# Optimization experiments

Measured on AMD Instinct MI355X. Metric: run time of the kernel, lower is better.

Reference implementation:

```python
import jax, jax.numpy as jnp
import numpy as np

KS, STRIDE, DIL = 5, 1, 1
PAD = (KS + (KS - 1) * (DIL - 1) - 1) // 2
EPS = 1e-5


def _unfold_t(x):
    # x: (N, C, T, V) -> (N, C, T_out, KS, V), zero-padded temporal windows
    N, C, T, V = x.shape
    xp = jnp.pad(x, ((0, 0), (0, 0), (PAD, PAD), (0, 0)))
    t_out = (T + 2 * PAD - DIL * (KS - 1) - 1) // STRIDE + 1
    idx = jnp.arange(t_out)[:, None] * STRIDE + jnp.arange(KS)[None, :] * DIL  # (T_out, KS)
    return xp[:, :, idx, :]


def _bn2d(x, g, b):
    # training-mode BatchNorm2d: biased batch stats over (N, T, V)
    mu = jnp.mean(x, axis=(0, 2, 3), keepdims=True)
    var = jnp.var(x, axis=(0, 2, 3), keepdims=True)
    xn = (x - mu) * jax.lax.rsqrt(var + EPS)
    return xn * g[None, :, None, None] + b[None, :, None, None]


def setup_inputs() -> dict:
    key = jax.random.key(0)
    ks = jax.random.split(key, 8)
    N, C, T, V = 64, 64, 128, 25
    R, O = 8, 128
    s = 0.05
    return {
        "x": jax.random.normal(ks[0], (N, C, T, V), jnp.float32),
        "Wv": jax.random.normal(ks[1], (R, C), jnp.float32) * s,
        "bv": jax.random.normal(ks[2], (R,), jnp.float32) * s,
        "Ww": jax.random.normal(ks[3], (KS * KS, KS), jnp.float32) * s,
        "bw": jax.random.normal(ks[4], (KS * KS,), jnp.float32) * s,
        "g_bn": jnp.ones((R,), jnp.float32),
        "b_bn": jnp.zeros((R,), jnp.float32),
        "Wr": jax.random.normal(ks[5], (R, C), jnp.float32) * s,
        "br": jax.random.normal(ks[6], (R,), jnp.float32) * s,
        "g_r": jnp.ones((R,), jnp.float32),
        "b_r": jnp.zeros((R,), jnp.float32),
        "Wo": jax.random.normal(ks[7], (O, R), jnp.float32) * s,
        "bo": jnp.zeros((O,), jnp.float32),
        "g_o": jnp.ones((O,), jnp.float32),
        "b_o": jnp.zeros((O,), jnp.float32),
    }


def reference(x, Wv, bv, Ww, bw, g_bn, b_bn, Wr, br, g_r, b_r, Wo, bo, g_o, b_o):
    N, C, T, V = x.shape
    # convV (1x1) then unfold both x and v
    v0 = jnp.einsum('rc,nctv->nrtv', Wv, x) + bv[None, :, None, None]
    xu = _unfold_t(x)      # (N, C, T, W, V)
    vu = _unfold_t(v0)     # (N, R, T, W, V)
    # mean over channels, move window dim to channel position for convW
    m = jnp.mean(xu, axis=1).transpose(0, 2, 1, 3)  # (N, W, T, V)
    w = jnp.einsum('ow,nwtv->notv', Ww, m) + bw[None, :, None, None]
    weights = jnp.tanh(w.reshape(N, KS, KS, T, V))  # (N, W, W, T, V)
    att = jnp.einsum('nwutv,nctuv->nctv', weights, vu)  # (N, R, T, V)
    # residual 1x1 conv + BN (in_channels != out_channels -> conv path)
    res = _bn2d(jnp.einsum('rc,nctv->nrtv', Wr, x) + br[None, :, None, None], g_r, b_r)
    h = _bn2d(att, g_bn, b_bn) + res
    h = jnp.where(h >= 0, h, 0.1 * h)  # LeakyReLU(0.1)
    out = _bn2d(jnp.einsum('or,nrtv->notv', Wo, h) + bo[None, :, None, None], g_o, b_o)
    return out
```

## Files before the change

kernel.cpp:

```cpp
#include <hip/hip_runtime.h>
#include <math.h>

#define TV 3200
#define NTV 204800
#define NB 400
constexpr float EPSF = 1e-5f;

template<int NS>
__device__ inline void partials2(const float (&vals)[NS], float* lds, float* out, int ncols){
  int lane = threadIdx.x & 63, wid = threadIdx.x >> 6;
  #pragma unroll
  for (int j = 0; j < NS; ++j){
    float v = vals[j];
    #pragma unroll
    for (int o = 32; o > 0; o >>= 1) v += __shfl_down(v, o);
    if (lane == 0) lds[j*2 + wid] = v;
  }
  __syncthreads();
  if ((int)threadIdx.x < NS)
    out[threadIdx.x*ncols + blockIdx.x] = lds[threadIdx.x*2] + lds[threadIdx.x*2 + 1];
}

__global__ __launch_bounds__(128, 2) void k_proj(
    const float* __restrict__ x, const float* __restrict__ Wv, const float* __restrict__ bv,
    const float* __restrict__ Wr, const float* __restrict__ br,
    float* __restrict__ v0, float* __restrict__ r0, float* __restrict__ s,
    float* __restrict__ pr){
  __shared__ __align__(16) float sW[1024];
  __shared__ float lds[32];
  const int tid = threadIdx.x;
  for (int i = tid; i < 1024; i += 128){
    int c = i >> 4, j = i & 15;
    sW[i] = (j < 8) ? Wv[j*64 + c] : Wr[(j-8)*64 + c];
  }
  __syncthreads();
  const int p4 = (blockIdx.x*128 + tid) * 4;
  const int n = p4 / TV, tv4 = p4 - n*TV;
  const float* xb = x + (size_t)n*64*TV + tv4;
  float4 av[8], ar[8];
  #pragma unroll
  for (int r = 0; r < 8; ++r){
    av[r] = make_float4(0.f,0.f,0.f,0.f);
    ar[r] = make_float4(0.f,0.f,0.f,0.f);
  }
  float4 ss = make_float4(0.f,0.f,0.f,0.f);
  #pragma unroll 8
  for (int c = 0; c < 64; ++c){
    float4 xv = *(const float4*)(xb + (size_t)c*TV);
    ss.x += xv.x; ss.y += xv.y; ss.z += xv.z; ss.w += xv.w;
    #pragma unroll
    for (int r = 0; r < 8; ++r){
      float wv = sW[c*16 + r], wr = sW[c*16 + 8 + r];
      av[r].x = fmaf(wv, xv.x, av[r].x); av[r].y = fmaf(wv, xv.y, av[r].y);
      av[r].z = fmaf(wv, xv.z, av[r].z); av[r].w = fmaf(wv, xv.w, av[r].w);
      ar[r].x = fmaf(wr, xv.x, ar[r].x); ar[r].y = fmaf(wr, xv.y, ar[r].y);
      ar[r].z = fmaf(wr, xv.z, ar[r].z); ar[r].w = fmaf(wr, xv.w, ar[r].w);
    }
  }
  *(float4*)(s + p4) = make_float4(ss.x*0.015625f, ss.y*0.015625f, ss.z*0.015625f, ss.w*0.015625f);
  float vals[16];
  #pragma unroll
  for (int r = 0; r < 8; ++r){
    float bvr = bv[r], brr = br[r];
    float4 vv = make_float4(av[r].x+bvr, av[r].y+bvr, av[r].z+bvr, av[r].w+bvr);
    *(float4*)(v0 + (size_t)r*NTV + p4) = vv;
    float4 rr = make_float4(ar[r].x+brr, ar[r].y+brr, ar[r].z+brr, ar[r].w+brr);
    *(float4*)(r0 + (size_t)r*NTV + p4) = rr;
    vals[r]   = rr.x + rr.y + rr.z + rr.w;
    vals[8+r] = rr.x*rr.x + rr.y*rr.y + rr.z*rr.z + rr.w*rr.w;
  }
  partials2<16>(vals, lds, pr, NB);
}

__global__ __launch_bounds__(128, 2) void k_att(
    const float* __restrict__ s, const float* __restrict__ Ww, const float* __restrict__ bw,
    const float* __restrict__ v0, float* __restrict__ att, float* __restrict__ patt){
  __shared__ __align__(16) float sS[616];
  __shared__ __align__(16) float sV[8*616];
  __shared__ float sWw[128], sbw[32];
  __shared__ float lds[32];
  const int tid = threadIdx.x;
  if (tid < 125) sWw[tid] = Ww[tid];
  if (tid < 25)  sbw[tid] = bw[tid];
  const int P0 = blockIdx.x * 512;
  const int base = P0 - 52;
  for (int i = tid; i < 154; i += 128){
    int q = base + i*4;
    float4 val;
    if (q >= 0 && q + 3 < NTV) val = *(const float4*)(s + q);
    else {
      float tmp[4];
      #pragma unroll
      for (int j = 0; j < 4; ++j){ int qe = q + j; tmp[j] = (qe >= 0 && qe < NTV) ? s[qe] : 0.f; }
      val = make_float4(tmp[0], tmp[1], tmp[2], tmp[3]);
    }
    *(float4*)&sS[i*4] = val;
  }
  for (int i = tid; i < 1232; i += 128){
    int r = i / 154, j = i - r*154;
    int q = base + j*4;
    const float* vr = v0 + (size_t)r*NTV;
    float4 val;
    if (q >= 0 && q + 3 < NTV) val = *(const float4*)(vr + q);
    else {
      float tmp[4];
      #pragma unroll
      for (int jj = 0; jj < 4; ++jj){ int qe = q + jj; tmp[jj] = (qe >= 0 && qe < NTV) ? vr[qe] : 0.f; }
      val = make_float4(tmp[0], tmp[1], tmp[2], tmp[3]);
    }
    *(float4*)&sV[r*616 + j*4] = val;
  }
  __syncthreads();
  float vals[16];
  #pragma unroll
  for (int j = 0; j < 16; ++j) vals[j] = 0.f;
  #pragma unroll
  for (int e = 0; e < 4; ++e){
    const int p = P0 + e*128 + tid;
    const int n = p / TV, tv = p - n*TV;
    const int li0 = e*128 + tid + 52;
    float m[5];
    #pragma unroll
    for (int k = 0; k < 5; ++k){
      int q = tv + (k-2)*25;
      m[k] = (q >= 0 && q < TV) ? sS[li0 + (k-2)*25] : 0.f;
    }
    float acc[8] = {0.f,0.f,0.f,0.f,0.f,0.f,0.f,0.f};
    #pragma unroll
    for (int u = 0; u < 5; ++u){
      float w2u = 0.f;
      #pragma unroll
      for (int w = 0; w < 5; ++w){
        int o = w*5 + u;
        float z = sbw[o];
        #pragma unroll
        for (int k = 0; k < 5; ++k) z = fmaf(sWw[o*5+k], m[k], z);
        w2u += tanhf(z);
      }
      int q = tv + (u-2)*25;
      if (q >= 0 && q < TV){
        int li = li0 + (u-2)*25;
        #pragma unroll
        for (int r = 0; r < 8; ++r) acc[r] = fmaf(w2u, sV[r*616 + li], acc[r]);
      }
    }
    #pragma unroll
    for (int r = 0; r < 8; ++r){
      att[(size_t)r*NTV + p] = acc[r];
      vals[r] += acc[r]; vals[8+r] += acc[r]*acc[r];
    }
  }
  partials2<16>(vals, lds, patt, NB);
}

__global__ __launch_bounds__(256) void k_bncoef(const float* __restrict__ pr,
    const float* __restrict__ patt,
    const float* __restrict__ g_bn, const float* __restrict__ b_bn,
    const float* __restrict__ g_r, const float* __restrict__ b_r,
    float* __restrict__ coef){
  __shared__ float lds[8];
  int b = blockIdx.x;
  bool isatt = (b >= 8);
  int r = b & 7;
  const float* ps = (isatt ? patt : pr) + r*NB;
  const float* pq = (isatt ? patt : pr) + (8+r)*NB;
  float s1 = 0.f, s2 = 0.f;
  for (int i = threadIdx.x; i < NB; i += 256){ s1 += ps[i]; s2 += pq[i]; }
  int lane = threadIdx.x & 63, wid = threadIdx.x >> 6;
  #pragma unroll
  for (int o = 32; o > 0; o >>= 1){ s1 += __shfl_down(s1, o); s2 += __shfl_down(s2, o); }
  if (lane == 0){ lds[wid] = s1; lds[4+wid] = s2; }
  __syncthreads();
  if (threadIdx.x == 0){
    float sum = lds[0]+lds[1]+lds[2]+lds[3];
    float sq  = lds[4]+lds[5]+lds[6]+lds[7];
    float mu  = sum / (float)NTV;
    float var = sq / (float)NTV - mu*mu;
    float g  = isatt ? g_bn[r] : g_r[r];
    float bb = isatt ? b_bn[r] : b_r[r];
    float a = g * rsqrtf(var + EPSF);
    int b0 = isatt ? 0 : 16;
    coef[b0 + r] = a;
    coef[b0 + 8 + r] = bb - a*mu;
  }
}

__global__ __launch_bounds__(128, 2) void k_h(
    const float* __restrict__ att, const float* __restrict__ r0,
    const float* __restrict__ coef, float* __restrict__ h, float* __restrict__ ph){
  __shared__ float sc[32];
  __shared__ float lds[96];
  const int tid = threadIdx.x;
  if (tid < 32) sc[tid] = coef[tid];
  __syncthreads();
  const int p4 = (blockIdx.x*128 + tid) * 4;
  float4 hv[8];
  float vals[44];
  #pragma unroll
  for (int r = 0; r < 8; ++r){
    float4 a = *(const float4*)(att + (size_t)r*NTV + p4);
    float4 b = *(const float4*)(r0  + (size_t)r*NTV + p4);
    float ca = sc[r], cb = sc[8+r], cc = sc[16+r], cd = sc[24+r];
    float4 z;
    z.x = ca*a.x + cb + cc*b.x + cd;
    z.y = ca*a.y + cb + cc*b.y + cd;
    z.z = ca*a.z + cb + cc*b.z + cd;
    z.w = ca*a.w + cb + cc*b.w + cd;
    hv[r].x = (z.x >= 0.f) ? z.x : 0.1f*z.x;
    hv[r].y = (z.y >= 0.f) ? z.y : 0.1f*z.y;
    hv[r].z = (z.z >= 0.f) ? z.z : 0.1f*z.z;
    hv[r].w = (z.w >= 0.f) ? z.w : 0.1f*z.w;
    *(float4*)(h + (size_t)r*NTV + p4) = hv[r];
    vals[r] = hv[r].x + hv[r].y + hv[r].z + hv[r].w;
  }
  int cnt = 8;
  #pragma unroll
  for (int r = 0; r < 8; ++r)
    #pragma unroll
    for (int r2 = r; r2 < 8; ++r2){
      vals[cnt++] = hv[r].x*hv[r2].x + hv[r].y*hv[r2].y + hv[r].z*hv[r2].z + hv[r].w*hv[r2].w;
    }
  partials2<44>(vals, lds, ph, NB);
}

__global__ __launch_bounds__(256) void k_foldred(const float* __restrict__ ph,
    const float* __restrict__ Wo, const float* __restrict__ bo,
    const float* __restrict__ g_o, const float* __restrict__ b_o,
    float* __restrict__ fold, float* __restrict__ bfold){
  __shared__ float sm[176];
  __shared__ float s44[44];
  __shared__ double muh[8];
  __shared__ double exx[64];
  const int tid = threadIdx.x;
  if (tid < 176){
    int j = tid >> 2, q = tid & 3;
    const float* row = ph + j*NB + q*100;
    float acc = 0.f;
    for (int i = 0; i < 100; ++i) acc += row[i];
    sm[tid] = acc;
  }
  __syncthreads();
  if (tid < 44) s44[tid] = sm[4*tid] + sm[4*tid+1] + sm[4*tid+2] + sm[4*tid+3];
  __syncthreads();
  if (tid < 8) muh[tid] = (double)s44[tid] / (double)NTV;
  if (tid == 0){
    int cnt = 8;
    for (int r = 0; r < 8; ++r)
      for (int r2 = r; r2 < 8; ++r2){
        double e = (double)s44[cnt++] / (double)NTV;
        exx[r*8+r2] = e; exx[r2*8+r] = e;
      }
  }
  __syncthreads();
  if (tid < 128){
    double w[8];
    #pragma unroll
    for (int r = 0; r < 8; ++r) w[r] = (double)Wo[tid*8+r];
    double bob = (double)bo[tid];
    double mu = bob;
    for (int r = 0; r < 8; ++r) mu += w[r]*muh[r];
    double t2 = 0.0;
    for (int r = 0; r < 8; ++r)
      for (int r2 = 0; r2 < 8; ++r2) t2 += w[r]*w[r2]*exx[r*8+r2];
    double ey2 = t2 + 2.0*bob*(mu - bob) + bob*bob;
    double var = ey2 - mu*mu;
    double a = (double)g_o[tid] / sqrt(var + (double)EPSF);
    #pragma unroll
    for (int r = 0; r < 8; ++r) fold[tid*8+r] = (float)(a * w[r]);
    bfold[tid] = (float)(a * (bob - mu) + (double)b_o[tid]);
  }
}

__global__ __launch_bounds__(256) void k_out(const float* __restrict__ h,
    const float* __restrict__ fold, const float* __restrict__ bfold,
    float* __restrict__ out){
  __shared__ float sW[256], sB[32];
  const int tid = threadIdx.x;
  const int yo = blockIdx.y * 32;
  sW[tid] = fold[yo*8 + tid];
  if (tid < 32) sB[tid] = bfold[yo + tid];
  __syncthreads();
  const int p4 = (blockIdx.x*256 + tid) * 4;
  const int n = p4 / TV, tv4 = p4 - n*TV;
  float4 hv[8];
  #pragma unroll
  for (int r = 0; r < 8; ++r) hv[r] = *(const float4*)(h + (size_t)r*NTV + p4);
  float* ob = out + (size_t)n*128*TV + tv4;
  #pragma unroll 4
  for (int o = 0; o < 32; ++o){
    float b = sB[o];
    float4 y = make_float4(b, b, b, b);
    #pragma unroll
    for (int r = 0; r < 8; ++r){
      float w = sW[o*8+r];
      y.x = fmaf(w, hv[r].x, y.x);
      y.y = fmaf(w, hv[r].y, y.y);
      y.z = fmaf(w, hv[r].z, y.z);
      y.w = fmaf(w, hv[r].w, y.w);
    }
    *(float4*)(ob + (size_t)(yo + o)*TV) = y;
  }
}

extern "C" void kernel_launch(void* const* d_in, const int* in_sizes, int n_in,
                              void* d_out, int out_size, void* d_ws, size_t ws_size,
                              hipStream_t stream){
  const float* x    = (const float*)d_in[0];
  const float* Wv   = (const float*)d_in[1];
  const float* bv   = (const float*)d_in[2];
  const float* Ww   = (const float*)d_in[3];
  const float* bw   = (const float*)d_in[4];
  const float* g_bn = (const float*)d_in[5];
  const float* b_bn = (const float*)d_in[6];
  const float* Wr   = (const float*)d_in[7];
  const float* br   = (const float*)d_in[8];
  const float* g_r  = (const float*)d_in[9];
  const float* b_r  = (const float*)d_in[10];
  const float* Wo   = (const float*)d_in[11];
  const float* bo   = (const float*)d_in[12];
  const float* g_o  = (const float*)d_in[13];
  const float* b_o  = (const float*)d_in[14];

  float* ws = (float*)d_ws;
  size_t off = 0;
  float* v0   = ws + off; off += 8*NTV;
  float* r0   = ws + off; off += 8*NTV;
  float* s    = ws + off; off += NTV;
  float* att  = ws + off; off += 8*NTV;
  float* hbuf = ws + off; off += 8*NTV;
  float* pr   = ws + off; off += 16*NB;
  float* patt = ws + off; off += 16*NB;
  float* ph   = ws + off; off += 44*NB;
  float* coef = ws + off; off += 32;
  float* fold = ws + off; off += 1024;
  float* bfold= ws + off; off += 128;

  k_proj   <<<NB, 128, 0, stream>>>(x, Wv, bv, Wr, br, v0, r0, s, pr);
  k_att    <<<NB, 128, 0, stream>>>(s, Ww, bw, v0, att, patt);
  k_bncoef <<<16, 256, 0, stream>>>(pr, patt, g_bn, b_bn, g_r, b_r, coef);
  k_h      <<<NB, 128, 0, stream>>>(att, r0, coef, hbuf, ph);
  k_foldred<<<1, 256, 0, stream>>>(ph, Wo, bo, g_o, b_o, fold, bfold);
  k_out    <<<dim3(200, 4), 256, 0, stream>>>(hbuf, fold, bfold, (float*)d_out);
}
```

Baseline: 262.8 us.

## Switch proj/att/h kernels to one point per thread with 256-thread blocks

Changes k_proj, k_att and k_h from four points per thread (float4) with 128-thread blocks to one scalar point per thread with 256-thread blocks, doubling the grid to 800 blocks. Partial-sum buffers and the fold reduction are resized to match. The aim is more threads in flight and better latency hiding on the many CUs. In exchange it gives up vectorised float4 loads, adds more partial reductions per point, and reloads halo data in k_att for smaller tiles.

```diff
diff --git a/kernel.cpp b/kernel.cpp
--- a/kernel.cpp
+++ b/kernel.cpp
@@ -3,154 +3,126 @@
 
 #define TV 3200
 #define NTV 204800
-#define NB 400
+#define NB 800
 constexpr float EPSF = 1e-5f;
 
 template<int NS>
-__device__ inline void partials2(const float (&vals)[NS], float* lds, float* out, int ncols){
+__device__ inline void partials(const float (&vals)[NS], float* lds, float* out, int ncols){
   int lane = threadIdx.x & 63, wid = threadIdx.x >> 6;
   #pragma unroll
   for (int j = 0; j < NS; ++j){
     float v = vals[j];
     #pragma unroll
     for (int o = 32; o > 0; o >>= 1) v += __shfl_down(v, o);
-    if (lane == 0) lds[j*2 + wid] = v;
+    if (lane == 0) lds[j*4 + wid] = v;
   }
   __syncthreads();
   if ((int)threadIdx.x < NS)
-    out[threadIdx.x*ncols + blockIdx.x] = lds[threadIdx.x*2] + lds[threadIdx.x*2 + 1];
-}
-
-__global__ __launch_bounds__(128, 2) void k_proj(
+    out[threadIdx.x*ncols + blockIdx.x] =
+      lds[threadIdx.x*4+0] + lds[threadIdx.x*4+1] + lds[threadIdx.x*4+2] + lds[threadIdx.x*4+3];
+}
+
+__global__ __launch_bounds__(256, 4) void k_proj(
     const float* __restrict__ x, const float* __restrict__ Wv, const float* __restrict__ bv,
     const float* __restrict__ Wr, const float* __restrict__ br,
     float* __restrict__ v0, float* __restrict__ r0, float* __restrict__ s,
     float* __restrict__ pr){
   __shared__ __align__(16) float sW[1024];
-  __shared__ float lds[32];
-  const int tid = threadIdx.x;
-  for (int i = tid; i < 1024; i += 128){
+  __shared__ float lds[64];
+  const int tid = threadIdx.x;
+  for (int i = tid; i < 1024; i += 256){
     int c = i >> 4, j = i & 15;
     sW[i] = (j < 8) ? Wv[j*64 + c] : Wr[(j-8)*64 + c];
   }
   __syncthreads();
-  const int p4 = (blockIdx.x*128 + tid) * 4;
-  const int n = p4 / TV, tv4 = p4 - n*TV;
-  const float* xb = x + (size_t)n*64*TV + tv4;
-  float4 av[8], ar[8];
-  #pragma unroll
-  for (int r = 0; r < 8; ++r){
-    av[r] = make_float4(0.f,0.f,0.f,0.f);
-    ar[r] = make_float4(0.f,0.f,0.f,0.f);
-  }
-  float4 ss = make_float4(0.f,0.f,0.f,0.f);
+  const int p = blockIdx.x*256 + tid;
+  const int n = p / TV, tv = p - n*TV;
+  const float* xp = x + (size_t)n*64*TV + tv;
+  float av[8] = {0,0,0,0,0,0,0,0};
+  float ar[8] = {0,0,0,0,0,0,0,0};
+  float ssum = 0.f;
   #pragma unroll 8
   for (int c = 0; c < 64; ++c){
-    float4 xv = *(const float4*)(xb + (size_t)c*TV);
-    ss.x += xv.x; ss.y += xv.y; ss.z += xv.z; ss.w += xv.w;
+    float xv = xp[(size_t)c*TV];
+    ssum += xv;
     #pragma unroll
     for (int r = 0; r < 8; ++r){
-      float wv = sW[c*16 + r], wr = sW[c*16 + 8 + r];
-      av[r].x = fmaf(wv, xv.x, av[r].x); av[r].y = fmaf(wv, xv.y, av[r].y);
-      av[r].z = fmaf(wv, xv.z, av[r].z); av[r].w = fmaf(wv, xv.w, av[r].w);
-      ar[r].x = fmaf(wr, xv.x, ar[r].x); ar[r].y = fmaf(wr, xv.y, ar[r].y);
-      ar[r].z = fmaf(wr, xv.z, ar[r].z); ar[r].w = fmaf(wr, xv.w, ar[r].w);
-    }
-  }
-  *(float4*)(s + p4) = make_float4(ss.x*0.015625f, ss.y*0.015625f, ss.z*0.015625f, ss.w*0.015625f);
+      av[r] = fmaf(sW[c*16 + r],     xv, av[r]);
+      ar[r] = fmaf(sW[c*16 + 8 + r], xv, ar[r]);
+    }
+  }
+  s[p] = ssum * 0.015625f;
   float vals[16];
   #pragma unroll
   for (int r = 0; r < 8; ++r){
-    float bvr = bv[r], brr = br[r];
-    float4 vv = make_float4(av[r].x+bvr, av[r].y+bvr, av[r].z+bvr, av[r].w+bvr);
-    *(float4*)(v0 + (size_t)r*NTV + p4) = vv;
-    float4 rr = make_float4(ar[r].x+brr, ar[r].y+brr, ar[r].z+brr, ar[r].w+brr);
-    *(float4*)(r0 + (size_t)r*NTV + p4) = rr;
-    vals[r]   = rr.x + rr.y + rr.z + rr.w;
-    vals[8+r] = rr.x*rr.x + rr.y*rr.y + rr.z*rr.z + rr.w*rr.w;
-  }
-  partials2<16>(vals, lds, pr, NB);
-}
-
-__global__ __launch_bounds__(128, 2) void k_att(
+    v0[(size_t)r*NTV + p] = av[r] + bv[r];
+    float rr = ar[r] + br[r];
+    r0[(size_t)r*NTV + p] = rr;
+    vals[r] = rr; vals[8+r] = rr*rr;
+  }
+  partials<16>(vals, lds, pr, NB);
+}
+
+__global__ __launch_bounds__(256, 4) void k_att(
     const float* __restrict__ s, const float* __restrict__ Ww, const float* __restrict__ bw,
     const float* __restrict__ v0, float* __restrict__ att, float* __restrict__ patt){
-  __shared__ __align__(16) float sS[616];
-  __shared__ __align__(16) float sV[8*616];
+  __shared__ float sS[360];
+  __shared__ float sV[8*360];
   __shared__ float sWw[128], sbw[32];
-  __shared__ float lds[32];
+  __shared__ float lds[64];
   const int tid = threadIdx.x;
   if (tid < 125) sWw[tid] = Ww[tid];
   if (tid < 25)  sbw[tid] = bw[tid];
-  const int P0 = blockIdx.x * 512;
+  const int P0 = blockIdx.x * 256;
   const int base = P0 - 52;
-  for (int i = tid; i < 154; i += 128){
-    int q = base + i*4;
-    float4 val;
-    if (q >= 0 && q + 3 < NTV) val = *(const float4*)(s + q);
-    else {
-      float tmp[4];
+  for (int i = tid; i < 360; i += 256){
+    int q = base + i;
+    sS[i] = (q >= 0 && q < NTV) ? s[q] : 0.f;
+  }
+  #pragma unroll
+  for (int r = 0; r < 8; ++r){
+    const float* vr = v0 + (size_t)r*NTV;
+    for (int i = tid; i < 360; i += 256){
+      int q = base + i;
+      sV[r*360 + i] = (q >= 0 && q < NTV) ? vr[q] : 0.f;
+    }
+  }
+  __syncthreads();
+  const int p = P0 + tid;
+  const int n = p / TV, tv = p - n*TV;
+  const int li = tid + 52;
+  float m[5];
+  #pragma unroll
+  for (int k = 0; k < 5; ++k){
+    int q = tv + (k-2)*25;
+    m[k] = (q >= 0 && q < TV) ? sS[li + (k-2)*25] : 0.f;
+  }
+  float acc[8] = {0,0,0,0,0,0,0,0};
+  #pragma unroll
+  for (int u = 0; u < 5; ++u){
+    float w2u = 0.f;
+    #pragma unroll
+    for (int w = 0; w < 5; ++w){
+      int o = w*5 + u;
+      float z = sbw[o];
       #pragma unroll
-      for (int j = 0; j < 4; ++j){ int qe = q + j; tmp[j] = (qe >= 0 && qe < NTV) ? s[qe] : 0.f; }
-      val = make_float4(tmp[0], tmp[1], tmp[2], tmp[3]);
-    }
-    *(float4*)&sS[i*4] = val;
-  }
-  for (int i = tid; i < 1232; i += 128){
-    int r = i / 154, j = i - r*154;
-    int q = base + j*4;
-    const float* vr = v0 + (size_t)r*NTV;
-    float4 val;
-    if (q >= 0 && q + 3 < NTV) val = *(const float4*)(vr + q);
-    else {
-      float tmp[4];
+      for (int k = 0; k < 5; ++k) z = fmaf(sWw[o*5+k], m[k], z);
+      w2u += tanhf(z);
+    }
+    int q = tv + (u-2)*25;
+    if (q >= 0 && q < TV){
+      int li2 = li + (u-2)*25;
       #pragma unroll
-      for (int jj = 0; jj < 4; ++jj){ int qe = q + jj; tmp[jj] = (qe >= 0 && qe < NTV) ? vr[qe] : 0.f; }
-      val = make_float4(tmp[0], tmp[1], tmp[2], tmp[3]);
-    }
-    *(float4*)&sV[r*616 + j*4] = val;
-  }
-  __syncthreads();
+      for (int r = 0; r < 8; ++r) acc[r] = fmaf(w2u, sV[r*360 + li2], acc[r]);
+    }
+  }
   float vals[16];
   #pragma unroll
-  for (int j = 0; j < 16; ++j) vals[j] = 0.f;
-  #pragma unroll
-  for (int e = 0; e < 4; ++e){
-    const int p = P0 + e*128 + tid;
-    const int n = p / TV, tv = p - n*TV;
-    const int li0 = e*128 + tid + 52;
-    float m[5];
-    #pragma unroll
-    for (int k = 0; k < 5; ++k){
-      int q = tv + (k-2)*25;
-      m[k] = (q >= 0 && q < TV) ? sS[li0 + (k-2)*25] : 0.f;
-    }
-    float acc[8] = {0.f,0.f,0.f,0.f,0.f,0.f,0.f,0.f};
-    #pragma unroll
-    for (int u = 0; u < 5; ++u){
-      float w2u = 0.f;
-      #pragma unroll
-      for (int w = 0; w < 5; ++w){
-        int o = w*5 + u;
-        float z = sbw[o];
-        #pragma unroll
-        for (int k = 0; k < 5; ++k) z = fmaf(sWw[o*5+k], m[k], z);
-        w2u += tanhf(z);
-      }
-      int q = tv + (u-2)*25;
-      if (q >= 0 && q < TV){
-        int li = li0 + (u-2)*25;
-        #pragma unroll
-        for (int r = 0; r < 8; ++r) acc[r] = fmaf(w2u, sV[r*616 + li], acc[r]);
-      }
-    }
-    #pragma unroll
-    for (int r = 0; r < 8; ++r){
-      att[(size_t)r*NTV + p] = acc[r];
-      vals[r] += acc[r]; vals[8+r] += acc[r]*acc[r];
-    }
-  }
-  partials2<16>(vals, lds, patt, NB);
+  for (int r = 0; r < 8; ++r){
+    att[(size_t)r*NTV + p] = acc[r];
+    vals[r] = acc[r]; vals[8+r] = acc[r]*acc[r];
+  }
+  partials<16>(vals, lds, patt, NB);
 }
 
 __global__ __launch_bounds__(256) void k_bncoef(const float* __restrict__ pr,
@@ -185,42 +157,32 @@
   }
 }
 
-__global__ __launch_bounds__(128, 2) void k_h(
+__global__ __launch_bounds__(256, 4) void k_h(
     const float* __restrict__ att, const float* __restrict__ r0,
     const float* __restrict__ coef, float* __restrict__ h, float* __restrict__ ph){
   __shared__ float sc[32];
-  __shared__ float lds[96];
+  __shared__ float lds[176];
   const int tid = threadIdx.x;
   if (tid < 32) sc[tid] = coef[tid];
   __syncthreads();
-  const int p4 = (blockIdx.x*128 + tid) * 4;
-  float4 hv[8];
+  const int p = blockIdx.x*256 + tid;
+  float hv[8];
   float vals[44];
   #pragma unroll
   for (int r = 0; r < 8; ++r){
-    float4 a = *(const float4*)(att + (size_t)r*NTV + p4);
-    float4 b = *(const float4*)(r0  + (size_t)r*NTV + p4);
-    float ca = sc[r], cb = sc[8+r], cc = sc[16+r], cd = sc[24+r];
-    float4 z;
-    z.x = ca*a.x + cb + cc*b.x + cd;
-    z.y = ca*a.y + cb + cc*b.y + cd;
-    z.z = ca*a.z + cb + cc*b.z + cd;
-    z.w = ca*a.w + cb + cc*b.w + cd;
-    hv[r].x = (z.x >= 0.f) ? z.x : 0.1f*z.x;
-    hv[r].y = (z.y >= 0.f) ? z.y : 0.1f*z.y;
-    hv[r].z = (z.z >= 0.f) ? z.z : 0.1f*z.z;
-    hv[r].w = (z.w >= 0.f) ? z.w : 0.1f*z.w;
-    *(float4*)(h + (size_t)r*NTV + p4) = hv[r];
-    vals[r] = hv[r].x + hv[r].y + hv[r].z + hv[r].w;
+    float a = att[(size_t)r*NTV + p];
+    float b = r0 [(size_t)r*NTV + p];
+    float z = sc[r]*a + sc[8+r] + sc[16+r]*b + sc[24+r];
+    hv[r] = (z >= 0.f) ? z : 0.1f*z;
+    h[(size_t)r*NTV + p] = hv[r];
+    vals[r] = hv[r];
   }
   int cnt = 8;
   #pragma unroll
   for (int r = 0; r < 8; ++r)
     #pragma unroll
-    for (int r2 = r; r2 < 8; ++r2){
-      vals[cnt++] = hv[r].x*hv[r2].x + hv[r].y*hv[r2].y + hv[r].z*hv[r2].z + hv[r].w*hv[r2].w;
-    }
-  partials2<44>(vals, lds, ph, NB);
+    for (int r2 = r; r2 < 8; ++r2) vals[cnt++] = hv[r]*hv[r2];
+  partials<44>(vals, lds, ph, NB);
 }
 
 __global__ __launch_bounds__(256) void k_foldred(const float* __restrict__ ph,
@@ -234,9 +196,9 @@
   const int tid = threadIdx.x;
   if (tid < 176){
     int j = tid >> 2, q = tid & 3;
-    const float* row = ph + j*NB + q*100;
+    const float* row = ph + j*NB + q*200;
     float acc = 0.f;
-    for (int i = 0; i < 100; ++i) acc += row[i];
+    for (int i = 0; i < 200; ++i) acc += row[i];
     sm[tid] = acc;
   }
   __syncthreads();
@@ -335,10 +297,10 @@
   float* fold = ws + off; off += 1024;
   float* bfold= ws + off; off += 128;
 
-  k_proj   <<<NB, 128, 0, stream>>>(x, Wv, bv, Wr, br, v0, r0, s, pr);
-  k_att    <<<NB, 128, 0, stream>>>(s, Ww, bw, v0, att, patt);
+  k_proj   <<<NB, 256, 0, stream>>>(x, Wv, bv, Wr, br, v0, r0, s, pr);
+  k_att    <<<NB, 256, 0, stream>>>(s, Ww, bw, v0, att, patt);
   k_bncoef <<<16, 256, 0, stream>>>(pr, patt, g_bn, b_bn, g_r, b_r, coef);
-  k_h      <<<NB, 128, 0, stream>>>(att, r0, coef, hbuf, ph);
+  k_h      <<<NB, 256, 0, stream>>>(att, r0, coef, hbuf, ph);
   k_foldred<<<1, 256, 0, stream>>>(ph, Wo, bo, g_o, b_o, fold, bfold);
   k_out    <<<dim3(200, 4), 256, 0, stream>>>(hbuf, fold, bfold, (float*)d_out);
 }
```

After: 253.4 us. -3.5%, faster.
